# Performance work log

Hardware: AMD Instinct MI355X
Metric: run time of the kernel (lower is better)

## Reference

```python
import jax, jax.numpy as jnp
import numpy as np

B, IN, H = 8192, 1024, 1024


def setup_inputs() -> dict:
    key = jax.random.key(0)
    ks = jax.random.split(key, 20)
    std = 1.0 / np.sqrt(H)
    u = lambda k, shape: jax.random.uniform(k, shape, jnp.float32, -std, std)
    inp = {
        "x": jax.random.normal(ks[0], (B, IN), jnp.float32),
        "hx": jax.random.normal(ks[1], (B, H), jnp.float32),
        "cx": jax.random.normal(ks[2], (B, H), jnp.float32),
        "task_id": 0,
        # x2h weights [H, IN] (torch Linear layout) and biases [H]
        "wxi": u(ks[3], (H, IN)), "bxi": u(ks[4], (H,)),
        "wxf": u(ks[5], (H, IN)), "bxf": u(ks[6], (H,)),
        "wxc": u(ks[7], (H, IN)), "bxc": u(ks[8], (H,)),
        "wxo": u(ks[9], (H, IN)), "bxo": u(ks[10], (H,)),
        # h2h weights [H, H] and biases [H]
        "whi": u(ks[11], (H, H)), "bhi": u(ks[12], (H,)),
        "whf": u(ks[13], (H, H)), "bhf": u(ks[14], (H,)),
        "whc": u(ks[15], (H, H)), "bhc": u(ks[16], (H,)),
        "who": u(ks[17], (H, H)), "bho": u(ks[18], (H,)),
    }
    return inp


def reference(x, hx, cx, task_id,
              wxi, bxi, wxf, bxf, wxc, bxc, wxo, bxo,
              whi, bhi, whf, bhf, whc, bhc, who, bho):
    # x = x.view(-1, x.size(1)) is identity for 2D input
    # gate pre-activations: Linear(x) + Linear(hx)  (torch: x @ W.T + b)
    ingate = x @ wxi.T + bxi + hx @ whi.T + bhi
    forgetgate = x @ wxf.T + bxf + hx @ whf.T + bhf
    cellgate = x @ wxc.T + bxc + hx @ whc.T + bhc
    outgate = x @ wxo.T + bxo + hx @ who.T + bho

    i = jax.nn.sigmoid(ingate)
    f = jax.nn.sigmoid(forgetgate)
    g = jnp.tanh(cellgate)
    o = jax.nn.sigmoid(outgate)

    cy = cx * f + i * g
    hy = o * jnp.tanh(cy)
    return hy, cy
```

## Files before the change

### kernel.cpp

```cpp
#include <hip/hip_runtime.h>
#include <hip/hip_bf16.h>

#define B_DIM  8192
#define IN_DIM 1024
#define H_DIM  1024
#define K_DIM  2048
#define BK     64
#define NT     (K_DIM / BK)

typedef __attribute__((ext_vector_type(8))) short bf16x8;
typedef __attribute__((ext_vector_type(4))) float f32x4;

__device__ __forceinline__ void mfma_16x16x32_bf16(f32x4& d, const bf16x8& a, const bf16x8& b) {
  asm volatile("v_mfma_f32_16x16x32_bf16 %0, %1, %2, %0" : "+v"(d) : "v"(a), "v"(b));
}

__device__ __forceinline__ void gload16(const void* g, void* l) {
  __builtin_amdgcn_global_load_lds(
      (const __attribute__((address_space(1))) void*)g,
      (__attribute__((address_space(3))) void*)l,
      16, 0, 0);
}

__device__ __forceinline__ float fast_sigmoid(float x) {
  return 1.0f / (1.0f + __expf(-x));
}
__device__ __forceinline__ float fast_tanh(float x) {
  float e = __expf(2.0f * x);
  return 1.0f - 2.0f / (e + 1.0f);
}

__global__ __launch_bounds__(256) void pack_a_kernel(
    const float* __restrict__ x, const float* __restrict__ hx,
    __hip_bfloat16* __restrict__ A) {
  const int idx = blockIdx.x * 256 + threadIdx.x;
  const int r  = idx >> 8;
  const int kk = (idx & 255) << 3;
  const float* src = (kk < IN_DIM) ? (x + (size_t)r * IN_DIM + kk)
                                   : (hx + (size_t)r * H_DIM + (kk - IN_DIM));
  const float4 v0 = ((const float4*)src)[0];
  const float4 v1 = ((const float4*)src)[1];
  __hip_bfloat16 t[8];
  t[0] = __float2bfloat16(v0.x); t[1] = __float2bfloat16(v0.y);
  t[2] = __float2bfloat16(v0.z); t[3] = __float2bfloat16(v0.w);
  t[4] = __float2bfloat16(v1.x); t[5] = __float2bfloat16(v1.y);
  t[6] = __float2bfloat16(v1.z); t[7] = __float2bfloat16(v1.w);
  *(uint4*)(A + ((size_t)idx << 3)) = *(const uint4*)t;
}

__global__ __launch_bounds__(256) void pack_w_kernel(
    const float* __restrict__ wxi, const float* __restrict__ wxf,
    const float* __restrict__ wxc, const float* __restrict__ wxo,
    const float* __restrict__ whi, const float* __restrict__ whf,
    const float* __restrict__ whc, const float* __restrict__ who,
    __hip_bfloat16* __restrict__ W) {
  const int idx = blockIdx.x * 256 + threadIdx.x;
  const int row = idx >> 8;
  const int kk  = (idx & 255) << 3;
  const int g = row >> 10, n = row & 1023;
  const float* src;
  if (kk < IN_DIM) {
    const float* p = (g == 0) ? wxi : (g == 1) ? wxf : (g == 2) ? wxc : wxo;
    src = p + (size_t)n * IN_DIM + kk;
  } else {
    const float* p = (g == 0) ? whi : (g == 1) ? whf : (g == 2) ? whc : who;
    src = p + (size_t)n * H_DIM + (kk - IN_DIM);
  }
  const float4 v0 = ((const float4*)src)[0];
  const float4 v1 = ((const float4*)src)[1];
  __hip_bfloat16 t[8];
  t[0] = __float2bfloat16(v0.x); t[1] = __float2bfloat16(v0.y);
  t[2] = __float2bfloat16(v0.z); t[3] = __float2bfloat16(v0.w);
  t[4] = __float2bfloat16(v1.x); t[5] = __float2bfloat16(v1.y);
  t[6] = __float2bfloat16(v1.z); t[7] = __float2bfloat16(v1.w);
  *(uint4*)(W + ((size_t)idx << 3)) = *(const uint4*)t;
}

__global__ __launch_bounds__(512, 2) void lstm_gemm_kernel(
    const __hip_bfloat16* __restrict__ A,
    const __hip_bfloat16* __restrict__ W,
    const float* __restrict__ cx,
    const float* __restrict__ bxi, const float* __restrict__ bhi,
    const float* __restrict__ bxf, const float* __restrict__ bhf,
    const float* __restrict__ bxc, const float* __restrict__ bhc,
    const float* __restrict__ bxo, const float* __restrict__ bho,
    float* __restrict__ hy, float* __restrict__ cy) {

  __shared__ __align__(16) char lds[2][64 * 1024];

  const int tid  = threadIdx.x;
  const int w    = tid >> 6;
  const int lane = tid & 63;
  const int wm = w >> 2, wn = w & 3;
  const int lq = lane >> 4, lr16 = lane & 15;

  const int bid = blockIdx.x;
  const int row0 = (bid & 31) * 256;
  const int col0 = (bid >> 5) * 64;

  const int srow = tid >> 3;
  const int scs  = (tid & 7) ^ (srow & 7);
  const __hip_bfloat16* Asrc = A + (size_t)(row0 + srow) * K_DIM + scs * 8;
  const __hip_bfloat16* Wsrc = W + (size_t)(col0 + srow) * K_DIM + scs * 8;
  const size_t Wg = (size_t)H_DIM * K_DIM;

  const int xr = lr16 & 7;
  const int aoff0 = wm * 16384 + lr16 * 128 + ((lq)     ^ xr) * 16;
  const int aoff1 = wm * 16384 + lr16 * 128 + ((4 + lq) ^ xr) * 16;
  const int woff0 = 32768 + (wn * 16 + lr16) * 128 + ((lq)     ^ xr) * 16;
  const int woff1 = 32768 + (wn * 16 + lr16) * 128 + ((4 + lq) ^ xr) * 16;

  f32x4 acc[4][8];
#pragma unroll
  for (int g = 0; g < 4; ++g)
#pragma unroll
    for (int m = 0; m < 8; ++m)
      acc[g][m] = (f32x4){0.f, 0.f, 0.f, 0.f};

#define STAGE_A(Q, KT)                                                        \
  {                                                                           \
    const size_t kof = (size_t)(KT) * BK;                                     \
    gload16(Asrc + kof,               &lds[Q][tid * 16]);                     \
    gload16(Asrc + 64 * K_DIM + kof,  &lds[Q][8192  + tid * 16]);             \
    gload16(Asrc + 128 * K_DIM + kof, &lds[Q][16384 + tid * 16]);             \
    gload16(Asrc + 192 * K_DIM + kof, &lds[Q][24576 + tid * 16]);             \
  }
#define STAGE_W(Q, KT)                                                        \
  {                                                                           \
    const size_t kof = (size_t)(KT) * BK;                                     \
    gload16(Wsrc + kof,          &lds[Q][32768 + tid * 16]);                  \
    gload16(Wsrc + Wg + kof,     &lds[Q][40960 + tid * 16]);                  \
    gload16(Wsrc + 2 * Wg + kof, &lds[Q][49152 + tid * 16]);                  \
    gload16(Wsrc + 3 * Wg + kof, &lds[Q][57344 + tid * 16]);                  \
  }

  STAGE_A(0, 0);
  STAGE_W(0, 0);
  asm volatile("s_waitcnt vmcnt(0)\n\ts_barrier" ::: "memory");

  bf16x8 af0[4][2], af1[4][2], wf01[2][2], wf23[2][2];
  {
    const char* rb = lds[0];
#pragma unroll
    for (int m = 0; m < 4; ++m) {
      af0[m][0] = *(const bf16x8*)(rb + aoff0 + m * 2048);
      af0[m][1] = *(const bf16x8*)(rb + aoff1 + m * 2048);
    }
#pragma unroll
    for (int gi = 0; gi < 2; ++gi) {
      wf01[gi][0] = *(const bf16x8*)(rb + woff0 + gi * 8192);
      wf01[gi][1] = *(const bf16x8*)(rb + woff1 + gi * 8192);
    }
  }

  for (int t = 0; t < NT; ++t) {
    const int p = t & 1, q = p ^ 1;
    const int tn1 = (t + 1 < NT) ? t + 1 : NT - 1;
    const char* rb = lds[p];
    const char* nb = lds[q];

#pragma unroll
    for (int gi = 0; gi < 2; ++gi) {
      wf23[gi][0] = *(const bf16x8*)(rb + woff0 + (2 + gi) * 8192);
      wf23[gi][1] = *(const bf16x8*)(rb + woff1 + (2 + gi) * 8192);
    }
    STAGE_A(q, tn1);
    STAGE_W(q, tn1);
    __builtin_amdgcn_s_setprio(1);
#pragma unroll
    for (int gi = 0; gi < 2; ++gi)
#pragma unroll
      for (int m = 0; m < 4; ++m) {
        mfma_16x16x32_bf16(acc[gi][m], af0[m][0], wf01[gi][0]);
        mfma_16x16x32_bf16(acc[gi][m], af0[m][1], wf01[gi][1]);
      }
    __builtin_amdgcn_s_setprio(0);

#pragma unroll
    for (int m = 0; m < 4; ++m) {
      af1[m][0] = *(const bf16x8*)(rb + aoff0 + 8192 + m * 2048);
      af1[m][1] = *(const bf16x8*)(rb + aoff1 + 8192 + m * 2048);
    }
    __builtin_amdgcn_s_setprio(1);
#pragma unroll
    for (int gi = 0; gi < 2; ++gi)
#pragma unroll
      for (int m = 0; m < 4; ++m) {
        mfma_16x16x32_bf16(acc[2 + gi][m], af0[m][0], wf23[gi][0]);
        mfma_16x16x32_bf16(acc[2 + gi][m], af0[m][1], wf23[gi][1]);
      }
    __builtin_amdgcn_s_setprio(0);

    __builtin_amdgcn_s_setprio(1);
#pragma unroll
    for (int gi = 0; gi < 2; ++gi)
#pragma unroll
      for (int m = 0; m < 4; ++m) {
        mfma_16x16x32_bf16(acc[gi][4 + m], af1[m][0], wf01[gi][0]);
        mfma_16x16x32_bf16(acc[gi][4 + m], af1[m][1], wf01[gi][1]);
      }
    __builtin_amdgcn_s_setprio(0);

    asm volatile("s_waitcnt vmcnt(0)\n\ts_barrier" ::: "memory");
#pragma unroll
    for (int m = 0; m < 4; ++m) {
      af0[m][0] = *(const bf16x8*)(nb + aoff0 + m * 2048);
      af0[m][1] = *(const bf16x8*)(nb + aoff1 + m * 2048);
    }
#pragma unroll
    for (int gi = 0; gi < 2; ++gi) {
      wf01[gi][0] = *(const bf16x8*)(nb + woff0 + gi * 8192);
      wf01[gi][1] = *(const bf16x8*)(nb + woff1 + gi * 8192);
    }
    __builtin_amdgcn_s_setprio(1);
#pragma unroll
    for (int gi = 0; gi < 2; ++gi)
#pragma unroll
      for (int m = 0; m < 4; ++m) {
        mfma_16x16x32_bf16(acc[2 + gi][4 + m], af1[m][0], wf23[gi][0]);
        mfma_16x16x32_bf16(acc[2 + gi][4 + m], af1[m][1], wf23[gi][1]);
      }
    __builtin_amdgcn_s_setprio(0);
    asm volatile("s_barrier" ::: "memory");
  }

  const int h = col0 + wn * 16 + lr16;
  const float bi  = bxi[h] + bhi[h];
  const float bff = bxf[h] + bhf[h];
  const float bc  = bxc[h] + bhc[h];
  const float bo  = bxo[h] + bho[h];
#pragma unroll
  for (int m = 0; m < 8; ++m) {
#pragma unroll
    for (int j = 0; j < 4; ++j) {
      const int r = row0 + wm * 128 + m * 16 + lq * 4 + j;
      const size_t o = (size_t)r * H_DIM + h;
      const float ig = fast_sigmoid(acc[0][m][j] + bi);
      const float fg = fast_sigmoid(acc[1][m][j] + bff);
      const float gg = fast_tanh   (acc[2][m][j] + bc);
      const float og = fast_sigmoid(acc[3][m][j] + bo);
      const float c  = cx[o] * fg + ig * gg;
      cy[o] = c;
      hy[o] = og * fast_tanh(c);
    }
  }
#undef STAGE_A
#undef STAGE_W
}

extern "C" void kernel_launch(void* const* d_in, const int* in_sizes, int n_in,
                              void* d_out, int out_size, void* d_ws, size_t ws_size,
                              hipStream_t stream) {
  const float* x   = (const float*)d_in[0];
  const float* hx  = (const float*)d_in[1];
  const float* cx  = (const float*)d_in[2];
  const float* wxi = (const float*)d_in[4];  const float* bxi = (const float*)d_in[5];
  const float* wxf = (const float*)d_in[6];  const float* bxf = (const float*)d_in[7];
  const float* wxc = (const float*)d_in[8];  const float* bxc = (const float*)d_in[9];
  const float* wxo = (const float*)d_in[10]; const float* bxo = (const float*)d_in[11];
  const float* whi = (const float*)d_in[12]; const float* bhi = (const float*)d_in[13];
  const float* whf = (const float*)d_in[14]; const float* bhf = (const float*)d_in[15];
  const float* whc = (const float*)d_in[16]; const float* bhc = (const float*)d_in[17];
  const float* who = (const float*)d_in[18]; const float* bho = (const float*)d_in[19];

  __hip_bfloat16* Abf = (__hip_bfloat16*)d_ws;
  __hip_bfloat16* Wbf = (__hip_bfloat16*)((char*)d_ws + (size_t)B_DIM * K_DIM * 2);

  float* hy  = (float*)d_out;
  float* cyo = (float*)d_out + (size_t)B_DIM * H_DIM;

  pack_a_kernel<<<(B_DIM * K_DIM / 8) / 256, 256, 0, stream>>>(x, hx, Abf);
  pack_w_kernel<<<(4 * H_DIM * K_DIM / 8) / 256, 256, 0, stream>>>(
      wxi, wxf, wxc, wxo, whi, whf, whc, who, Wbf);

  lstm_gemm_kernel<<<dim3(512), 512, 0, stream>>>(
      Abf, Wbf, cx, bxi, bhi, bxf, bhf, bxc, bhc, bxo, bho, hy, cyo);
}
```

Measured before the change: 163.8 us.

## Load weight fragments directly into registers, halving LDS footprint

Weight tiles are no longer staged through LDS. Each wave now loads its MFMA B-fragments straight from global memory into registers, with two register sets swapped across a 2-way unrolled K loop. The A tile stays in double-buffered LDS, which halves LDS usage per block and removes the LDS round trip and bank pressure for weights. The cost is that the weight global loads are no longer shared across the two wm waves, so the same weight data is fetched twice from L2. It also raises VGPR usage and uses less coalesced 16-byte per-lane loads.

```diff
diff --git a/kernel.cpp b/kernel.cpp
--- a/kernel.cpp
+++ b/kernel.cpp
@@ -86,7 +86,7 @@
     const float* __restrict__ bxo, const float* __restrict__ bho,
     float* __restrict__ hy, float* __restrict__ cy) {
 
-  __shared__ __align__(16) char lds[2][64 * 1024];
+  __shared__ __align__(16) char lds[2][32 * 1024];
 
   const int tid  = threadIdx.x;
   const int w    = tid >> 6;
@@ -101,14 +101,14 @@
   const int srow = tid >> 3;
   const int scs  = (tid & 7) ^ (srow & 7);
   const __hip_bfloat16* Asrc = A + (size_t)(row0 + srow) * K_DIM + scs * 8;
-  const __hip_bfloat16* Wsrc = W + (size_t)(col0 + srow) * K_DIM + scs * 8;
+
   const size_t Wg = (size_t)H_DIM * K_DIM;
+  const __hip_bfloat16* Wfrag =
+      W + (size_t)(col0 + wn * 16 + lr16) * K_DIM + lq * 8;
 
   const int xr = lr16 & 7;
   const int aoff0 = wm * 16384 + lr16 * 128 + ((lq)     ^ xr) * 16;
   const int aoff1 = wm * 16384 + lr16 * 128 + ((4 + lq) ^ xr) * 16;
-  const int woff0 = 32768 + (wn * 16 + lr16) * 128 + ((lq)     ^ xr) * 16;
-  const int woff1 = 32768 + (wn * 16 + lr16) * 128 + ((4 + lq) ^ xr) * 16;
 
   f32x4 acc[4][8];
 #pragma unroll
@@ -125,103 +125,72 @@
     gload16(Asrc + 128 * K_DIM + kof, &lds[Q][16384 + tid * 16]);             \
     gload16(Asrc + 192 * K_DIM + kof, &lds[Q][24576 + tid * 16]);             \
   }
-#define STAGE_W(Q, KT)                                                        \
+#define LOAD_W(DST, KT)                                                       \
   {                                                                           \
     const size_t kof = (size_t)(KT) * BK;                                     \
-    gload16(Wsrc + kof,          &lds[Q][32768 + tid * 16]);                  \
-    gload16(Wsrc + Wg + kof,     &lds[Q][40960 + tid * 16]);                  \
-    gload16(Wsrc + 2 * Wg + kof, &lds[Q][49152 + tid * 16]);                  \
-    gload16(Wsrc + 3 * Wg + kof, &lds[Q][57344 + tid * 16]);                  \
-  }
+    _Pragma("unroll")                                                         \
+    for (int g = 0; g < 4; ++g) {                                             \
+      DST[g][0] = *(const bf16x8*)(Wfrag + (size_t)g * Wg + kof);             \
+      DST[g][1] = *(const bf16x8*)(Wfrag + (size_t)g * Wg + kof + 32);        \
+    }                                                                         \
+  }
+#define TILE_COMPUTE(P, WF)                                                   \
+  {                                                                           \
+    const char* rb = lds[P];                                                  \
+    bf16x8 af0[4][2], af1[4][2];                                              \
+    _Pragma("unroll")                                                         \
+    for (int m = 0; m < 4; ++m) {                                             \
+      af0[m][0] = *(const bf16x8*)(rb + aoff0 + m * 2048);                    \
+      af0[m][1] = *(const bf16x8*)(rb + aoff1 + m * 2048);                    \
+    }                                                                         \
+    __builtin_amdgcn_s_setprio(1);                                            \
+    _Pragma("unroll")                                                         \
+    for (int g = 0; g < 4; ++g)                                               \
+      _Pragma("unroll")                                                       \
+      for (int m = 0; m < 4; ++m) {                                           \
+        mfma_16x16x32_bf16(acc[g][m], af0[m][0], WF[g][0]);                   \
+        mfma_16x16x32_bf16(acc[g][m], af0[m][1], WF[g][1]);                   \
+      }                                                                       \
+    __builtin_amdgcn_s_setprio(0);                                            \
+    _Pragma("unroll")                                                         \
+    for (int m = 0; m < 4; ++m) {                                             \
+      af1[m][0] = *(const bf16x8*)(rb + aoff0 + 8192 + m * 2048);             \
+      af1[m][1] = *(const bf16x8*)(rb + aoff1 + 8192 + m * 2048);             \
+    }                                                                         \
+    __builtin_amdgcn_s_setprio(1);                                            \
+    _Pragma("unroll")                                                         \
+    for (int g = 0; g < 4; ++g)                                               \
+      _Pragma("unroll")                                                       \
+      for (int m = 0; m < 4; ++m) {                                           \
+        mfma_16x16x32_bf16(acc[g][4 + m], af1[m][0], WF[g][0]);               \
+        mfma_16x16x32_bf16(acc[g][4 + m], af1[m][1], WF[g][1]);               \
+      }                                                                       \
+    __builtin_amdgcn_s_setprio(0);                                            \
+  }
+#define SYNC()  asm volatile("s_waitcnt vmcnt(0)\n\ts_barrier" ::: "memory")
+
+  bf16x8 wfA[4][2], wfB[4][2];
 
   STAGE_A(0, 0);
-  STAGE_W(0, 0);
-  asm volatile("s_waitcnt vmcnt(0)\n\ts_barrier" ::: "memory");
-
-  bf16x8 af0[4][2], af1[4][2], wf01[2][2], wf23[2][2];
-  {
-    const char* rb = lds[0];
-#pragma unroll
-    for (int m = 0; m < 4; ++m) {
-      af0[m][0] = *(const bf16x8*)(rb + aoff0 + m * 2048);
-      af0[m][1] = *(const bf16x8*)(rb + aoff1 + m * 2048);
+  LOAD_W(wfA, 0);
+  SYNC();
+
+#pragma unroll 1
+  for (int t = 0; t < NT; t += 2) {
+    {
+      const int tn = (t + 1 < NT) ? t + 1 : NT - 1;
+      STAGE_A(1, tn);
+      LOAD_W(wfB, tn);
+      TILE_COMPUTE(0, wfA);
+      SYNC();
     }
-#pragma unroll
-    for (int gi = 0; gi < 2; ++gi) {
-      wf01[gi][0] = *(const bf16x8*)(rb + woff0 + gi * 8192);
-      wf01[gi][1] = *(const bf16x8*)(rb + woff1 + gi * 8192);
+    {
+      const int tn = (t + 2 < NT) ? t + 2 : NT - 1;
+      STAGE_A(0, tn);
+      LOAD_W(wfA, tn);
+      TILE_COMPUTE(1, wfB);
+      SYNC();
     }
-  }
-
-  for (int t = 0; t < NT; ++t) {
-    const int p = t & 1, q = p ^ 1;
-    const int tn1 = (t + 1 < NT) ? t + 1 : NT - 1;
-    const char* rb = lds[p];
-    const char* nb = lds[q];
-
-#pragma unroll
-    for (int gi = 0; gi < 2; ++gi) {
-      wf23[gi][0] = *(const bf16x8*)(rb + woff0 + (2 + gi) * 8192);
-      wf23[gi][1] = *(const bf16x8*)(rb + woff1 + (2 + gi) * 8192);
-    }
-    STAGE_A(q, tn1);
-    STAGE_W(q, tn1);
-    __builtin_amdgcn_s_setprio(1);
-#pragma unroll
-    for (int gi = 0; gi < 2; ++gi)
-#pragma unroll
-      for (int m = 0; m < 4; ++m) {
-        mfma_16x16x32_bf16(acc[gi][m], af0[m][0], wf01[gi][0]);
-        mfma_16x16x32_bf16(acc[gi][m], af0[m][1], wf01[gi][1]);
-      }
-    __builtin_amdgcn_s_setprio(0);
-
-#pragma unroll
-    for (int m = 0; m < 4; ++m) {
-      af1[m][0] = *(const bf16x8*)(rb + aoff0 + 8192 + m * 2048);
-      af1[m][1] = *(const bf16x8*)(rb + aoff1 + 8192 + m * 2048);
-    }
-    __builtin_amdgcn_s_setprio(1);
-#pragma unroll
-    for (int gi = 0; gi < 2; ++gi)
-#pragma unroll
-      for (int m = 0; m < 4; ++m) {
-        mfma_16x16x32_bf16(acc[2 + gi][m], af0[m][0], wf23[gi][0]);
-        mfma_16x16x32_bf16(acc[2 + gi][m], af0[m][1], wf23[gi][1]);
-      }
-    __builtin_amdgcn_s_setprio(0);
-
-    __builtin_amdgcn_s_setprio(1);
-#pragma unroll
-    for (int gi = 0; gi < 2; ++gi)
-#pragma unroll
-      for (int m = 0; m < 4; ++m) {
-        mfma_16x16x32_bf16(acc[gi][4 + m], af1[m][0], wf01[gi][0]);
-        mfma_16x16x32_bf16(acc[gi][4 + m], af1[m][1], wf01[gi][1]);
-      }
-    __builtin_amdgcn_s_setprio(0);
-
-    asm volatile("s_waitcnt vmcnt(0)\n\ts_barrier" ::: "memory");
-#pragma unroll
-    for (int m = 0; m < 4; ++m) {
-      af0[m][0] = *(const bf16x8*)(nb + aoff0 + m * 2048);
-      af0[m][1] = *(const bf16x8*)(nb + aoff1 + m * 2048);
-    }
-#pragma unroll
-    for (int gi = 0; gi < 2; ++gi) {
-      wf01[gi][0] = *(const bf16x8*)(nb + woff0 + gi * 8192);
-      wf01[gi][1] = *(const bf16x8*)(nb + woff1 + gi * 8192);
-    }
-    __builtin_amdgcn_s_setprio(1);
-#pragma unroll
-    for (int gi = 0; gi < 2; ++gi)
-#pragma unroll
-      for (int m = 0; m < 4; ++m) {
-        mfma_16x16x32_bf16(acc[2 + gi][4 + m], af1[m][0], wf23[gi][0]);
-        mfma_16x16x32_bf16(acc[2 + gi][4 + m], af1[m][1], wf23[gi][1]);
-      }
-    __builtin_amdgcn_s_setprio(0);
-    asm volatile("s_barrier" ::: "memory");
   }
 
   const int h = col0 + wn * 16 + lr16;
@@ -245,7 +214,9 @@
     }
   }
 #undef STAGE_A
-#undef STAGE_W
+#undef LOAD_W
+#undef TILE_COMPUTE
+#undef SYNC
 }
 
 extern "C" void kernel_launch(void* const* d_in, const int* in_sizes, int n_in,
```

After: 221.8 us. 35.4% more time.

## Split global-to-LDS staging into four phases interleaved with MFMA clusters and swizzle blocks

Applied to the files above, without the earlier changes.

Replaces the bulk A/W prefetch with four smaller staged loads spread across the four MFMA clusters of each K step. Partial vmcnt(4) waits and extra barriers keep at most two load groups in flight, so the per-step vmcnt(0) drain goes away. A single A-fragment register set is reused instead of two, which lowers register pressure. Block indices are also remapped so that consecutive blocks share weight column tiles, for better L2 locality. The risk is the subtle ordering of waits and barriers: a wrong count could race on the double-buffered LDS, and the extra barriers add sync cost.

```diff
diff --git a/kernel.cpp b/kernel.cpp
--- a/kernel.cpp
+++ b/kernel.cpp
@@ -95,8 +95,9 @@
   const int lq = lane >> 4, lr16 = lane & 15;
 
   const int bid = blockIdx.x;
-  const int row0 = (bid & 31) * 256;
-  const int col0 = (bid >> 5) * 64;
+  const int swz = (bid & 7) * 64 + (bid >> 3);
+  const int row0 = (swz & 31) * 256;
+  const int col0 = (swz >> 5) * 64;
 
   const int srow = tid >> 3;
   const int scs  = (tid & 7) ^ (srow & 7);
@@ -117,112 +118,116 @@
     for (int m = 0; m < 8; ++m)
       acc[g][m] = (f32x4){0.f, 0.f, 0.f, 0.f};
 
-#define STAGE_A(Q, KT)                                                        \
+#define STAGE_U1(Q, KT)                                                       \
   {                                                                           \
     const size_t kof = (size_t)(KT) * BK;                                     \
     gload16(Asrc + kof,               &lds[Q][tid * 16]);                     \
+    gload16(Asrc + 128 * K_DIM + kof, &lds[Q][16384 + tid * 16]);             \
+  }
+#define STAGE_U4(Q, KT)                                                       \
+  {                                                                           \
+    const size_t kof = (size_t)(KT) * BK;                                     \
     gload16(Asrc + 64 * K_DIM + kof,  &lds[Q][8192  + tid * 16]);             \
-    gload16(Asrc + 128 * K_DIM + kof, &lds[Q][16384 + tid * 16]);             \
     gload16(Asrc + 192 * K_DIM + kof, &lds[Q][24576 + tid * 16]);             \
   }
-#define STAGE_W(Q, KT)                                                        \
+#define STAGE_U2(Q, KT)                                                       \
   {                                                                           \
     const size_t kof = (size_t)(KT) * BK;                                     \
     gload16(Wsrc + kof,          &lds[Q][32768 + tid * 16]);                  \
     gload16(Wsrc + Wg + kof,     &lds[Q][40960 + tid * 16]);                  \
+  }
+#define STAGE_U3(Q, KT)                                                       \
+  {                                                                           \
+    const size_t kof = (size_t)(KT) * BK;                                     \
     gload16(Wsrc + 2 * Wg + kof, &lds[Q][49152 + tid * 16]);                  \
     gload16(Wsrc + 3 * Wg + kof, &lds[Q][57344 + tid * 16]);                  \
   }
-
-  STAGE_A(0, 0);
-  STAGE_W(0, 0);
-  asm volatile("s_waitcnt vmcnt(0)\n\ts_barrier" ::: "memory");
-
-  bf16x8 af0[4][2], af1[4][2], wf01[2][2], wf23[2][2];
-  {
-    const char* rb = lds[0];
+#define WAIT4_BAR() asm volatile("s_waitcnt vmcnt(4)\n\ts_barrier" ::: "memory")
+#define BAR()       asm volatile("s_barrier" ::: "memory")
+
+  STAGE_U1(0, 0);
+  STAGE_U2(0, 0);
+  STAGE_U3(0, 0);
+  STAGE_U4(0, 0);
+  WAIT4_BAR();
+
+  bf16x8 af[4][2], wf01[2][2], wf23[2][2];
+
+  for (int t = 0; t < NT; ++t) {
+    const int p = t & 1, q = p ^ 1;
+    const int tn = (t + 1 < NT) ? t + 1 : NT - 1;
+    const char* rb = lds[p];
+
 #pragma unroll
     for (int m = 0; m < 4; ++m) {
-      af0[m][0] = *(const bf16x8*)(rb + aoff0 + m * 2048);
-      af0[m][1] = *(const bf16x8*)(rb + aoff1 + m * 2048);
+      af[m][0] = *(const bf16x8*)(rb + aoff0 + m * 2048);
+      af[m][1] = *(const bf16x8*)(rb + aoff1 + m * 2048);
     }
 #pragma unroll
     for (int gi = 0; gi < 2; ++gi) {
       wf01[gi][0] = *(const bf16x8*)(rb + woff0 + gi * 8192);
       wf01[gi][1] = *(const bf16x8*)(rb + woff1 + gi * 8192);
     }
-  }
-
-  for (int t = 0; t < NT; ++t) {
-    const int p = t & 1, q = p ^ 1;
-    const int tn1 = (t + 1 < NT) ? t + 1 : NT - 1;
-    const char* rb = lds[p];
-    const char* nb = lds[q];
+    STAGE_U1(q, tn);
+    WAIT4_BAR();
+    __builtin_amdgcn_s_setprio(1);
+#pragma unroll
+    for (int gi = 0; gi < 2; ++gi)
+#pragma unroll
+      for (int m = 0; m < 4; ++m) {
+        mfma_16x16x32_bf16(acc[gi][m], af[m][0], wf01[gi][0]);
+        mfma_16x16x32_bf16(acc[gi][m], af[m][1], wf01[gi][1]);
+      }
+    __builtin_amdgcn_s_setprio(0);
 
 #pragma unroll
     for (int gi = 0; gi < 2; ++gi) {
       wf23[gi][0] = *(const bf16x8*)(rb + woff0 + (2 + gi) * 8192);
       wf23[gi][1] = *(const bf16x8*)(rb + woff1 + (2 + gi) * 8192);
     }
-    STAGE_A(q, tn1);
-    STAGE_W(q, tn1);
-    __builtin_amdgcn_s_setprio(1);
-#pragma unroll
-    for (int gi = 0; gi < 2; ++gi)
-#pragma unroll
-      for (int m = 0; m < 4; ++m) {
-        mfma_16x16x32_bf16(acc[gi][m], af0[m][0], wf01[gi][0]);
-        mfma_16x16x32_bf16(acc[gi][m], af0[m][1], wf01[gi][1]);
+    STAGE_U2(q, tn);
+    WAIT4_BAR();
+    __builtin_amdgcn_s_setprio(1);
+#pragma unroll
+    for (int gi = 0; gi < 2; ++gi)
+#pragma unroll
+      for (int m = 0; m < 4; ++m) {
+        mfma_16x16x32_bf16(acc[2 + gi][m], af[m][0], wf23[gi][0]);
+        mfma_16x16x32_bf16(acc[2 + gi][m], af[m][1], wf23[gi][1]);
       }
     __builtin_amdgcn_s_setprio(0);
 
 #pragma unroll
     for (int m = 0; m < 4; ++m) {
-      af1[m][0] = *(const bf16x8*)(rb + aoff0 + 8192 + m * 2048);
-      af1[m][1] = *(const bf16x8*)(rb + aoff1 + 8192 + m * 2048);
-    }
-    __builtin_amdgcn_s_setprio(1);
-#pragma unroll
-    for (int gi = 0; gi < 2; ++gi)
-#pragma unroll
-      for (int m = 0; m < 4; ++m) {
-        mfma_16x16x32_bf16(acc[2 + gi][m], af0[m][0], wf23[gi][0]);
-        mfma_16x16x32_bf16(acc[2 + gi][m], af0[m][1], wf23[gi][1]);
-      }
-    __builtin_amdgcn_s_setprio(0);
-
-    __builtin_amdgcn_s_setprio(1);
-#pragma unroll
-    for (int gi = 0; gi < 2; ++gi)
-#pragma unroll
-      for (int m = 0; m < 4; ++m) {
-        mfma_16x16x32_bf16(acc[gi][4 + m], af1[m][0], wf01[gi][0]);
-        mfma_16x16x32_bf16(acc[gi][4 + m], af1[m][1], wf01[gi][1]);
-      }
-    __builtin_amdgcn_s_setprio(0);
-
-    asm volatile("s_waitcnt vmcnt(0)\n\ts_barrier" ::: "memory");
-#pragma unroll
-    for (int m = 0; m < 4; ++m) {
-      af0[m][0] = *(const bf16x8*)(nb + aoff0 + m * 2048);
-      af0[m][1] = *(const bf16x8*)(nb + aoff1 + m * 2048);
-    }
-#pragma unroll
-    for (int gi = 0; gi < 2; ++gi) {
-      wf01[gi][0] = *(const bf16x8*)(nb + woff0 + gi * 8192);
-      wf01[gi][1] = *(const bf16x8*)(nb + woff1 + gi * 8192);
-    }
-    __builtin_amdgcn_s_setprio(1);
-#pragma unroll
-    for (int gi = 0; gi < 2; ++gi)
-#pragma unroll
-      for (int m = 0; m < 4; ++m) {
-        mfma_16x16x32_bf16(acc[2 + gi][4 + m], af1[m][0], wf23[gi][0]);
-        mfma_16x16x32_bf16(acc[2 + gi][4 + m], af1[m][1], wf23[gi][1]);
-      }
-    __builtin_amdgcn_s_setprio(0);
-    asm volatile("s_barrier" ::: "memory");
-  }
+      af[m][0] = *(const bf16x8*)(rb + aoff0 + 8192 + m * 2048);
+      af[m][1] = *(const bf16x8*)(rb + aoff1 + 8192 + m * 2048);
+    }
+    STAGE_U3(q, tn);
+    BAR();
+    __builtin_amdgcn_s_setprio(1);
+#pragma unroll
+    for (int gi = 0; gi < 2; ++gi)
+#pragma unroll
+      for (int m = 0; m < 4; ++m) {
+        mfma_16x16x32_bf16(acc[2 + gi][4 + m], af[m][0], wf23[gi][0]);
+        mfma_16x16x32_bf16(acc[2 + gi][4 + m], af[m][1], wf23[gi][1]);
+      }
+    __builtin_amdgcn_s_setprio(0);
+
+    STAGE_U4(q, tn);
+    WAIT4_BAR();
+    __builtin_amdgcn_s_setprio(1);
+#pragma unroll
+    for (int gi = 0; gi < 2; ++gi)
+#pragma unroll
+      for (int m = 0; m < 4; ++m) {
+        mfma_16x16x32_bf16(acc[gi][4 + m], af[m][0], wf01[gi][0]);
+        mfma_16x16x32_bf16(acc[gi][4 + m], af[m][1], wf01[gi][1]);
+      }
+    __builtin_amdgcn_s_setprio(0);
+  }
+
+  asm volatile("s_waitcnt vmcnt(0)" ::: "memory");
 
   const int h = col0 + wn * 16 + lr16;
   const float bi  = bxi[h] + bhi[h];
@@ -244,8 +249,12 @@
       hy[o] = og * fast_tanh(c);
     }
   }
-#undef STAGE_A
-#undef STAGE_W
+#undef STAGE_U1
+#undef STAGE_U2
+#undef STAGE_U3
+#undef STAGE_U4
+#undef WAIT4_BAR
+#undef BAR
 }
 
 extern "C" void kernel_launch(void* const* d_in, const int* in_sizes, int n_in,
```

Result: faster. 158.9 us (-3.0%).
